# Kernel optimization log

Measured on AMD Instinct MI355X. Metric: run time of the kernel, lower is better.

Reference implementation:

```python
import jax, jax.numpy as jnp
import numpy as np

N = 50000      # nodes
E = 1600000    # edges (avg degree 32)
D_IN = 128
HID = 64


def setup_inputs() -> dict:
    key = jax.random.key(0)
    ks = jax.random.split(key, 7)
    x = jax.random.normal(ks[0], (N, D_IN), dtype=jnp.float32)
    ei = jax.random.randint(ks[1], (2, E), 0, N, dtype=jnp.int32)
    ew = jax.random.uniform(ks[2], (E,), dtype=jnp.float32)
    # GCNConv linear weights (glorot-ish scale); lin has no bias, conv bias added post-aggregation
    W1 = jax.random.normal(ks[3], (HID, D_IN), dtype=jnp.float32) * (1.0 / np.sqrt(D_IN))
    b1 = jnp.zeros((HID,), dtype=jnp.float32)
    W2 = jax.random.normal(ks[4], (HID, HID), dtype=jnp.float32) * (1.0 / np.sqrt(HID))
    b2 = jnp.zeros((HID,), dtype=jnp.float32)
    return {"x": x, "ei": ei, "ew": ew, "W1": W1, "b1": b1, "W2": W2, "b2": b2}


def _gcn_conv(x, src, dst, ew_all, W, b, n_nodes):
    """PyG GCNConv: gcn_norm (self-loops already appended) + x@W.T, gather-scale-scatter, +b."""
    deg = jax.ops.segment_sum(ew_all, dst, num_segments=n_nodes)  # dst-side weighted degree
    dinv = jnp.where(deg > 0, jax.lax.rsqrt(deg), 0.0)            # deg^{-1/2}, inf->0
    norm = dinv[src] * ew_all * dinv[dst]                          # [E+N]
    h = x @ W.T                                                    # [N, hid]
    msg = h[src] * norm[:, None]                                   # gather + scale
    out = jax.ops.segment_sum(msg, dst, num_segments=n_nodes)     # scatter-add
    return out + b


def reference(x, ei, ew, W1, b1, W2, b2):
    n_nodes = x.shape[0]
    # add self loops once (fill value 1.0), shared by both conv layers
    loop = jnp.arange(n_nodes, dtype=ei.dtype)
    src = jnp.concatenate([ei[0], loop])
    dst = jnp.concatenate([ei[1], loop])
    ew_all = jnp.concatenate([ew, jnp.ones((n_nodes,), dtype=ew.dtype)])

    h1 = jax.nn.relu(_gcn_conv(x, src, dst, ew_all, W1, b1, n_nodes))
    # dropout is identity in eval mode
    h2 = _gcn_conv(h1, src, dst, ew_all, W2, b2, n_nodes)
    return h2 + h1
```

## Files before the change

kernel.cpp:

```cpp
#include <hip/hip_runtime.h>

#define HID 64
#define DIN 128
#define NBLK 512
#define CSH 14
#define CAP (1 << CSH)
#define PAD 68

typedef unsigned long long ull;
typedef unsigned short u16;

static __device__ __forceinline__ u16 f2bf(float f) {
  unsigned u = __float_as_uint(f);
  unsigned lsb = (u >> 16) & 1u;
  u += 0x7fffu + lsb;
  return (u16)(u >> 16);
}


template <int K, int NT, bool XT_PRELOADED>
__device__ __forceinline__ void gemm_tile(const float* __restrict__ X,
                                          const float* __restrict__ W,
                                          u16* __restrict__ out,
                                          float* XT, float* WL,
                                          int n0, int n_nodes, int tid) {
  constexpr int ROWS = NT / 8;
  const int tx = tid & 15;
  const int ty = tid >> 4;
  float acc[2][4] = {{0.f}};

  for (int ph = 0; ph < K / 64; ++ph) {
    const int d0 = ph * 64;
    __syncthreads();
    if (!XT_PRELOADED) {
#pragma unroll
      for (int k = 0; k < 2; ++k) {
        int f = tid + k * NT;
        int r = f >> 4, q = f & 15;
        int n = n0 + r;
        float4 xv = (n < n_nodes)
          ? *reinterpret_cast<const float4*>(&X[(size_t)n * K + d0 + 4 * q])
          : make_float4(0.f, 0.f, 0.f, 0.f);
        *reinterpret_cast<float4*>(&XT[r * PAD + 4 * q]) = xv;
      }
    }
#pragma unroll
    for (int k = 0; k < 1024 / NT; ++k) {
      int gq = tid + k * NT;
      int qd = gq >> 6, j = gq & 63;
      float4 wv = *reinterpret_cast<const float4*>(&W[(size_t)j * K + d0 + 4 * qd]);
      WL[(4 * qd + 0) * PAD + j] = wv.x;
      WL[(4 * qd + 1) * PAD + j] = wv.y;
      WL[(4 * qd + 2) * PAD + j] = wv.z;
      WL[(4 * qd + 3) * PAD + j] = wv.w;
    }
    __syncthreads();
#pragma unroll 4
    for (int dd = 0; dd < 64; dd += 4) {
      float4 ws[4];
#pragma unroll
      for (int dk = 0; dk < 4; ++dk)
        ws[dk] = *reinterpret_cast<const float4*>(&WL[(dd + dk) * PAD + 4 * tx]);
      float4 x0 = *reinterpret_cast<const float4*>(&XT[ty * PAD + dd]);
      float4 x1 = *reinterpret_cast<const float4*>(&XT[(ty + ROWS / 2) * PAD + dd]);
      float xm0[4] = {x0.x, x0.y, x0.z, x0.w};
      float xm1[4] = {x1.x, x1.y, x1.z, x1.w};
#pragma unroll
      for (int dk = 0; dk < 4; ++dk) {
        acc[0][0] = fmaf(xm0[dk], ws[dk].x, acc[0][0]);
        acc[0][1] = fmaf(xm0[dk], ws[dk].y, acc[0][1]);
        acc[0][2] = fmaf(xm0[dk], ws[dk].z, acc[0][2]);
        acc[0][3] = fmaf(xm0[dk], ws[dk].w, acc[0][3]);
        acc[1][0] = fmaf(xm1[dk], ws[dk].x, acc[1][0]);
        acc[1][1] = fmaf(xm1[dk], ws[dk].y, acc[1][1]);
        acc[1][2] = fmaf(xm1[dk], ws[dk].z, acc[1][2]);
        acc[1][3] = fmaf(xm1[dk], ws[dk].w, acc[1][3]);
      }
    }
  }

#pragma unroll
  for (int mi = 0; mi < 2; ++mi) {
    int n = n0 + mi * (ROWS / 2) + ty;
    if (n < n_nodes) {
      ushort4 o = make_ushort4(f2bf(acc[mi][0]), f2bf(acc[mi][1]),
                               f2bf(acc[mi][2]), f2bf(acc[mi][3]));
      *reinterpret_cast<ushort4*>(&out[(size_t)n * HID + 4 * tx]) = o;
    }
  }
}


__global__ __launch_bounds__(512) void k_build_gemm(const int* __restrict__ src,
                                                    const int* __restrict__ dst,
                                                    const float* __restrict__ ew,
                                                    int* __restrict__ cursor,
                                                    int2* __restrict__ bufA,
                                                    int E, int chunk,
                                                    const float* __restrict__ x,
                                                    const float* __restrict__ W1,
                                                    u16* __restrict__ h,
                                                    int n_nodes) {
  __shared__ float S[2 * 64 * PAD];
  int b = blockIdx.x, tid = threadIdx.x;
  if (b >= NBLK) {
    gemm_tile<DIN, 512, false>(x, W1, h, S, S + 64 * PAD, (b - NBLK) * 64, n_nodes, tid);
    return;
  }
  int* h0   = (int*)S;
  int* h1_  = (int*)S + 256;
  int* cur0 = (int*)S + 512;
  int* cur1 = (int*)S + 768;
  if (tid < 256) { h0[tid] = 0; h1_[tid] = 0; }
  __syncthreads();
  int e0 = b * chunk, e1 = min(E, e0 + chunk);
  const int half = tid >> 8;
  int* hh = half ? h1_ : h0;
  int4 s4[2], d4[2];
  float4 w4[2];
  bool val[2];
#pragma unroll
  for (int it = 0; it < 2; ++it) {
    int e = e0 + 4 * tid + it * 2048;
    val[it] = (e < e1);
    if (val[it]) {
      s4[it] = *reinterpret_cast<const int4*>(&src[e]);
      d4[it] = *reinterpret_cast<const int4*>(&dst[e]);
      w4[it] = *reinterpret_cast<const float4*>(&ew[e]);
      atomicAdd(&hh[d4[it].x >> 8], 1);
      atomicAdd(&hh[d4[it].y >> 8], 1);
      atomicAdd(&hh[d4[it].z >> 8], 1);
      atomicAdd(&hh[d4[it].w >> 8], 1);
    }
  }
  for (int e = e0 + 4096 + 4 * tid; e < e1; e += 2048) {
    int4 dd = *reinterpret_cast<const int4*>(&dst[e]);
    atomicAdd(&hh[dd.x >> 8], 1);
    atomicAdd(&hh[dd.y >> 8], 1);
    atomicAdd(&hh[dd.z >> 8], 1);
    atomicAdd(&hh[dd.w >> 8], 1);
  }
  __syncthreads();
  if (tid < 256) {
    int c0 = h0[tid], c1 = h1_[tid], tot = c0 + c1;
    int ofs = (tot > 0) ? atomicAdd(&cursor[tid], tot) : 0;
    cur0[tid] = (tid << CSH) + ofs;
    cur1[tid] = (tid << CSH) + ofs + c0;
  }
  __syncthreads();
  int* cc = half ? cur1 : cur0;
#pragma unroll
  for (int it = 0; it < 2; ++it) {
    if (val[it]) {
      int p0 = atomicAdd(&cc[d4[it].x >> 8], 1);
      bufA[p0] = make_int2(__float_as_int(w4[it].x),
                           (int)(((unsigned)s4[it].x << 16) | (unsigned)d4[it].x));
      int p1 = atomicAdd(&cc[d4[it].y >> 8], 1);
      bufA[p1] = make_int2(__float_as_int(w4[it].y),
                           (int)(((unsigned)s4[it].y << 16) | (unsigned)d4[it].y));
      int p2 = atomicAdd(&cc[d4[it].z >> 8], 1);
      bufA[p2] = make_int2(__float_as_int(w4[it].z),
                           (int)(((unsigned)s4[it].z << 16) | (unsigned)d4[it].z));
      int p3 = atomicAdd(&cc[d4[it].w >> 8], 1);
      bufA[p3] = make_int2(__float_as_int(w4[it].w),
                           (int)(((unsigned)s4[it].w << 16) | (unsigned)d4[it].w));
    }
  }
  for (int e = e0 + 4096 + 4 * tid; e < e1; e += 2048) {
    int4 ss = *reinterpret_cast<const int4*>(&src[e]);
    int4 dd = *reinterpret_cast<const int4*>(&dst[e]);
    float4 ww = *reinterpret_cast<const float4*>(&ew[e]);
    int p0 = atomicAdd(&cc[dd.x >> 8], 1);
    bufA[p0] = make_int2(__float_as_int(ww.x), (int)(((unsigned)ss.x << 16) | (unsigned)dd.x));
    int p1 = atomicAdd(&cc[dd.y >> 8], 1);
    bufA[p1] = make_int2(__float_as_int(ww.y), (int)(((unsigned)ss.y << 16) | (unsigned)dd.y));
    int p2 = atomicAdd(&cc[dd.z >> 8], 1);
    bufA[p2] = make_int2(__float_as_int(ww.z), (int)(((unsigned)ss.z << 16) | (unsigned)dd.z));
    int p3 = atomicAdd(&cc[dd.w >> 8], 1);
    bufA[p3] = make_int2(__float_as_int(ww.w), (int)(((unsigned)ss.w << 16) | (unsigned)dd.w));
  }
}


__global__ __launch_bounds__(1024) void k_passB(const int2* __restrict__ bufA,
                                                const int* __restrict__ cursor,
                                                int2* __restrict__ bufB,
                                                int* __restrict__ offs,
                                                int* __restrict__ cnt,
                                                float* __restrict__ dinv,
                                                int NBC, int N) {
  int bin = blockIdx.x, tid = threadIdx.x;
  __shared__ int h2[256];
  __shared__ int cur[256];
  __shared__ float dg[256];
  int bbase = bin << CSH;
  int m = cursor[bin];
  if (tid < 256) { h2[tid] = 0; dg[tid] = 0.f; }
  __syncthreads();
  int2 rloc[16];
#pragma unroll
  for (int k = 0; k < 16; ++k) {
    int i = tid + k * 1024;
    if (i < m) {
      rloc[k] = bufA[bbase + i];
      atomicAdd(&h2[(unsigned)rloc[k].y & 255u], 1);
    }
  }
  __syncthreads();
  int own = (tid < 256) ? h2[tid] : 0;
  for (int o = 1; o < 256; o <<= 1) {
    int u = 0;
    if (tid < 256 && tid >= o) u = h2[tid - o];
    __syncthreads();
    if (tid < 256) h2[tid] += u;
    __syncthreads();
  }
  int nd = (bin << 8) + tid;
  if (tid < 256) {
    int excl = h2[tid] - own;
    cur[tid] = excl;
    if (nd < N) { offs[nd] = bbase + excl; cnt[nd] = own; }
  }
  __syncthreads();
#pragma unroll
  for (int k = 0; k < 16; ++k) {
    int i = tid + k * 1024;
    if (i < m) {
      int2 r = rloc[k];
      unsigned sd = (unsigned)r.y;
      int dl = (int)(sd & 255u);
      int p = atomicAdd(&cur[dl], 1);
      bufB[bbase + p] = make_int2(r.x, (int)(sd >> 16));
      atomicAdd(&dg[dl], __int_as_float(r.x));
    }
  }
  __syncthreads();
  if (tid < 256 && nd < N) dinv[nd] = rsqrtf(1.0f + dg[tid]);
}


__device__ __forceinline__ void bfma8(const uint4& v, float w, float* a) {
  a[0] = fmaf(__uint_as_float(v.x << 16), w, a[0]);
  a[1] = fmaf(__uint_as_float(v.x & 0xffff0000u), w, a[1]);
  a[2] = fmaf(__uint_as_float(v.y << 16), w, a[2]);
  a[3] = fmaf(__uint_as_float(v.y & 0xffff0000u), w, a[3]);
  a[4] = fmaf(__uint_as_float(v.z << 16), w, a[4]);
  a[5] = fmaf(__uint_as_float(v.z & 0xffff0000u), w, a[5]);
  a[6] = fmaf(__uint_as_float(v.w << 16), w, a[6]);
  a[7] = fmaf(__uint_as_float(v.w & 0xffff0000u), w, a[7]);
}

__device__ __forceinline__ void agg_node(const u16* __restrict__ h,
                                         const int2* __restrict__ recs,
                                         const float* __restrict__ dinv,
                                         int beg, int end, int node, float di,
                                         int lane, int p8, float* r) {
  float a[8], b[8];
  {
    uint4 v = *reinterpret_cast<const uint4*>(&h[(size_t)node * HID + p8]);
    a[0] = __uint_as_float(v.x << 16) * di;
    a[1] = __uint_as_float(v.x & 0xffff0000u) * di;
    a[2] = __uint_as_float(v.y << 16) * di;
    a[3] = __uint_as_float(v.y & 0xffff0000u) * di;
    a[4] = __uint_as_float(v.z << 16) * di;
    a[5] = __uint_as_float(v.z & 0xffff0000u) * di;
    a[6] = __uint_as_float(v.w << 16) * di;
    a[7] = __uint_as_float(v.w & 0xffff0000u) * di;
#pragma unroll
    for (int j = 0; j < 8; ++j) b[j] = 0.f;
  }

  const int gb = lane & 56;
  const int l7 = lane & 7;
  int i = beg;
  if (i + 8 <= end) {
    ull rr = *reinterpret_cast<const ull*>(&recs[i + l7]);
    float dv = dinv[(int)(rr >> 32)];
    for (;;) {
      float wd = __uint_as_float((unsigned)rr) * dv;
      ull ru = (rr & 0xffffffff00000000ull) | (ull)__float_as_uint(wd);
      bool more = (i + 16 <= end);
      ull rr_n = 0; float dv_n = 0.f;
      if (more) {
        rr_n = *reinterpret_cast<const ull*>(&recs[i + 8 + l7]);
        dv_n = dinv[(int)(rr_n >> 32)];
      }
#pragma unroll
      for (int k = 0; k < 8; ++k) {
        ull q = __shfl(ru, gb | k, 64);
        float wk = __uint_as_float((unsigned)q);
        int sk = (int)(q >> 32);
        uint4 vk = *reinterpret_cast<const uint4*>(&h[(size_t)sk * HID + p8]);
        bfma8(vk, wk, (k & 1) ? b : a);
      }
      i += 8;
      if (!more) break;
      rr = rr_n; dv = dv_n;
    }
  }
  if (i + 4 <= end) {
    int2 r0 = recs[i];     int2 r1 = recs[i + 1];
    int2 r2 = recs[i + 2]; int2 r3 = recs[i + 3];
    uint4 v0 = *reinterpret_cast<const uint4*>(&h[(size_t)r0.y * HID + p8]);
    uint4 v1 = *reinterpret_cast<const uint4*>(&h[(size_t)r1.y * HID + p8]);
    uint4 v2 = *reinterpret_cast<const uint4*>(&h[(size_t)r2.y * HID + p8]);
    uint4 v3 = *reinterpret_cast<const uint4*>(&h[(size_t)r3.y * HID + p8]);
    bfma8(v0, __int_as_float(r0.x) * dinv[r0.y], a);
    bfma8(v1, __int_as_float(r1.x) * dinv[r1.y], b);
    bfma8(v2, __int_as_float(r2.x) * dinv[r2.y], a);
    bfma8(v3, __int_as_float(r3.x) * dinv[r3.y], b);
    i += 4;
  }
  if (i + 2 <= end) {
    int2 r0 = recs[i];     int2 r1 = recs[i + 1];
    uint4 v0 = *reinterpret_cast<const uint4*>(&h[(size_t)r0.y * HID + p8]);
    uint4 v1 = *reinterpret_cast<const uint4*>(&h[(size_t)r1.y * HID + p8]);
    bfma8(v0, __int_as_float(r0.x) * dinv[r0.y], a);
    bfma8(v1, __int_as_float(r1.x) * dinv[r1.y], b);
    i += 2;
  }
  if (i < end) {
    int2 r0 = recs[i];
    uint4 v0 = *reinterpret_cast<const uint4*>(&h[(size_t)r0.y * HID + p8]);
    bfma8(v0, __int_as_float(r0.x) * dinv[r0.y], a);
  }
#pragma unroll
  for (int j = 0; j < 8; ++j) r[j] = (a[j] + b[j]) * di;
}


__global__ __launch_bounds__(256) void k_agg_gemm(const u16* __restrict__ h,
                                                  const int2* __restrict__ recs,
                                                  const int* __restrict__ offs,
                                                  const int* __restrict__ cnt,
                                                  const float* __restrict__ dinv,
                                                  const float* __restrict__ bias,
                                                  const float* __restrict__ W2,
                                                  float* __restrict__ h1,
                                                  u16* __restrict__ h2,
                                                  int n_nodes) {
  __shared__ float S[(32 + 64) * PAD];
  float* XT = S;
  float* WL = S + 32 * PAD;
  int tid = threadIdx.x;
  int lane = tid & 63;
  int p8 = (lane & 7) * 8;
  int nl = (tid >> 6) * 8 + (lane >> 3);
  int node = blockIdx.x * 32 + nl;
  if (node < n_nodes) {
    float di = dinv[node];
    float r[8];
    agg_node(h, recs, dinv, offs[node], offs[node] + cnt[node], node, di,
             lane, p8, r);
    float4 bb0 = *reinterpret_cast<const float4*>(&bias[p8]);
    float4 bb1 = *reinterpret_cast<const float4*>(&bias[p8 + 4]);
    r[0] += bb0.x; r[1] += bb0.y; r[2] += bb0.z; r[3] += bb0.w;
    r[4] += bb1.x; r[5] += bb1.y; r[6] += bb1.z; r[7] += bb1.w;
#pragma unroll
    for (int j = 0; j < 8; ++j) r[j] = fmaxf(r[j], 0.f);
    float4 lo = make_float4(r[0], r[1], r[2], r[3]);
    float4 hi = make_float4(r[4], r[5], r[6], r[7]);
    *reinterpret_cast<float4*>(&h1[(size_t)node * HID + p8]) = lo;
    *reinterpret_cast<float4*>(&h1[(size_t)node * HID + p8 + 4]) = hi;
    *reinterpret_cast<float4*>(&XT[nl * PAD + p8]) = lo;
    *reinterpret_cast<float4*>(&XT[nl * PAD + p8 + 4]) = hi;
  }
  gemm_tile<HID, 256, true>(nullptr, W2, h2, XT, WL, blockIdx.x * 32, n_nodes, tid);
}


__global__ __launch_bounds__(256) void k_agg2(const u16* __restrict__ h,
                                              const int2* __restrict__ recs,
                                              const int* __restrict__ offs,
                                              const int* __restrict__ cnt,
                                              const float* __restrict__ dinv,
                                              const float* __restrict__ bias,
                                              const float* __restrict__ resid,
                                              float* __restrict__ out, int n_nodes) {
  int tid = threadIdx.x;
  int lane = tid & 63;
  int p8 = (lane & 7) * 8;
  int node = (blockIdx.x * 4 + (tid >> 6)) * 8 + (lane >> 3);
  if (node >= n_nodes) return;
  float di = dinv[node];
  float r[8];
  agg_node(h, recs, dinv, offs[node], offs[node] + cnt[node], node, di,
           lane, p8, r);
  float4 bb0 = *reinterpret_cast<const float4*>(&bias[p8]);
  float4 bb1 = *reinterpret_cast<const float4*>(&bias[p8 + 4]);
  float4 rs0 = *reinterpret_cast<const float4*>(&resid[(size_t)node * HID + p8]);
  float4 rs1 = *reinterpret_cast<const float4*>(&resid[(size_t)node * HID + p8 + 4]);
  r[0] += bb0.x + rs0.x; r[1] += bb0.y + rs0.y;
  r[2] += bb0.z + rs0.z; r[3] += bb0.w + rs0.w;
  r[4] += bb1.x + rs1.x; r[5] += bb1.y + rs1.y;
  r[6] += bb1.z + rs1.z; r[7] += bb1.w + rs1.w;
  *reinterpret_cast<float4*>(&out[(size_t)node * HID + p8]) =
      make_float4(r[0], r[1], r[2], r[3]);
  *reinterpret_cast<float4*>(&out[(size_t)node * HID + p8 + 4]) =
      make_float4(r[4], r[5], r[6], r[7]);
}


extern "C" void kernel_launch(void* const* d_in, const int* in_sizes, int n_in,
                              void* d_out, int out_size, void* d_ws, size_t ws_size,
                              hipStream_t stream) {
  const float* x  = (const float*)d_in[0];
  const int*   ei = (const int*)d_in[1];
  const float* ew = (const float*)d_in[2];
  const float* W1 = (const float*)d_in[3];
  const float* b1 = (const float*)d_in[4];
  const float* W2 = (const float*)d_in[5];
  const float* b2 = (const float*)d_in[6];
  float* out = (float*)d_out;

  const int N = in_sizes[0] / DIN;
  const int E = in_sizes[2];
  const int* src = ei;
  const int* dst = ei + E;

  const int NBC = (N + 255) >> 8;
  const int chunk = (((E + NBLK - 1) / NBLK) + 3) & ~3;
  const int nslab = NBC << CSH;

  char* p = (char*)d_ws;
  auto carve = [&](size_t bytes) {
    char* r = p;
    p += (bytes + 255) & ~(size_t)255;
    return r;
  };
  int*   cursor = (int*)carve(256 * 4);
  int*   offs   = (int*)carve((size_t)N * 4);
  int*   cnt    = (int*)carve((size_t)N * 4);
  float* dinv   = (float*)carve((size_t)N * 4);
  int2*  bufA   = (int2*)carve((size_t)nslab * 8);
  int2*  bufB   = (int2*)carve((size_t)nslab * 8);
  u16*   h      = (u16*)carve((size_t)N * HID * 2);
  u16*   h2     = (u16*)carve((size_t)N * HID * 2);
  float* h1     = (float*)carve((size_t)N * HID * 4);

  int gblk  = (N + 63) / 64;
  int gblk2 = (N + 31) / 32;
  int ablk  = (N + 31) / 32;

  hipMemsetAsync(cursor, 0, 256 * 4, stream);
  k_build_gemm<<<NBLK + gblk, 512, 0, stream>>>(src, dst, ew, cursor, bufA, E, chunk,
                                                x, W1, h, N);
  k_passB<<<NBC, 1024, 0, stream>>>(bufA, cursor, bufB, offs, cnt, dinv, NBC, N);
  k_agg_gemm<<<gblk2, 256, 0, stream>>>(h, bufB, offs, cnt, dinv, b1, W2, h1, h2, N);
  k_agg2<<<ablk, 256, 0, stream>>>(h2, bufB, offs, cnt, dinv, b2, h1, out, N);
}
```

Baseline: 209.9 us.

## Stage bucketed edge scatter through LDS for coalesced global writes

The build kernel now sorts each block's first 4096 edges by coarse bucket in shared memory, then writes them to bufA in contiguous runs. Edges beyond the first 4096 in a chunk fall back to per-edge global atomics. Pass B now sorts records by fine bucket in LDS in chunks of 4096 before writing bufB, so stores are coalesced instead of scattered. It also computes degrees during the histogram pass. The extra LDS passes, scans and syncs are the price paid to remove random global stores.

```diff
diff --git a/kernel.cpp b/kernel.cpp
--- a/kernel.cpp
+++ b/kernel.cpp
@@ -101,83 +101,84 @@
                                                     const float* __restrict__ W1,
                                                     u16* __restrict__ h,
                                                     int n_nodes) {
-  __shared__ float S[2 * 64 * PAD];
+  __shared__ float S[9216];
   int b = blockIdx.x, tid = threadIdx.x;
   if (b >= NBLK) {
     gemm_tile<DIN, 512, false>(x, W1, h, S, S + 64 * PAD, (b - NBLK) * 64, n_nodes, tid);
     return;
   }
-  int* h0   = (int*)S;
-  int* h1_  = (int*)S + 256;
-  int* cur0 = (int*)S + 512;
-  int* cur1 = (int*)S + 768;
-  if (tid < 256) { h0[tid] = 0; h1_[tid] = 0; }
+  int2* lbuf  = (int2*)S;
+  int*  lhist = (int*)&S[8192];
+  int*  lstart= (int*)&S[8448];
+  int*  lcur  = (int*)&S[8704];
+  int*  gofs  = (int*)&S[8960];
+  if (tid < 256) lhist[tid] = 0;
   __syncthreads();
   int e0 = b * chunk, e1 = min(E, e0 + chunk);
-  const int half = tid >> 8;
-  int* hh = half ? h1_ : h0;
+  int m = e1 - e0;
   int4 s4[2], d4[2];
   float4 w4[2];
   bool val[2];
 #pragma unroll
   for (int it = 0; it < 2; ++it) {
-    int e = e0 + 4 * tid + it * 2048;
-    val[it] = (e < e1);
+    int e = e0 + 4 * (tid + it * 512);
+    val[it] = (e < e1) && (e < e0 + 4096);
     if (val[it]) {
       s4[it] = *reinterpret_cast<const int4*>(&src[e]);
       d4[it] = *reinterpret_cast<const int4*>(&dst[e]);
       w4[it] = *reinterpret_cast<const float4*>(&ew[e]);
-      atomicAdd(&hh[d4[it].x >> 8], 1);
-      atomicAdd(&hh[d4[it].y >> 8], 1);
-      atomicAdd(&hh[d4[it].z >> 8], 1);
-      atomicAdd(&hh[d4[it].w >> 8], 1);
-    }
-  }
-  for (int e = e0 + 4096 + 4 * tid; e < e1; e += 2048) {
-    int4 dd = *reinterpret_cast<const int4*>(&dst[e]);
-    atomicAdd(&hh[dd.x >> 8], 1);
-    atomicAdd(&hh[dd.y >> 8], 1);
-    atomicAdd(&hh[dd.z >> 8], 1);
-    atomicAdd(&hh[dd.w >> 8], 1);
-  }
-  __syncthreads();
+      atomicAdd(&lhist[d4[it].x >> 8], 1);
+      atomicAdd(&lhist[d4[it].y >> 8], 1);
+      atomicAdd(&lhist[d4[it].z >> 8], 1);
+      atomicAdd(&lhist[d4[it].w >> 8], 1);
+    }
+  }
+  __syncthreads();
+  int own = (tid < 256) ? lhist[tid] : 0;
+  for (int o = 1; o < 256; o <<= 1) {
+    int u = 0;
+    if (tid < 256 && tid >= o) u = lhist[tid - o];
+    __syncthreads();
+    if (tid < 256) lhist[tid] += u;
+    __syncthreads();
+  }
   if (tid < 256) {
-    int c0 = h0[tid], c1 = h1_[tid], tot = c0 + c1;
-    int ofs = (tot > 0) ? atomicAdd(&cursor[tid], tot) : 0;
-    cur0[tid] = (tid << CSH) + ofs;
-    cur1[tid] = (tid << CSH) + ofs + c0;
-  }
-  __syncthreads();
-  int* cc = half ? cur1 : cur0;
+    int excl = lhist[tid] - own;
+    lstart[tid] = excl;
+    lcur[tid] = excl;
+    int g = (own > 0) ? atomicAdd(&cursor[tid], own) : 0;
+    gofs[tid] = (tid << CSH) + g - excl;
+  }
+  __syncthreads();
 #pragma unroll
   for (int it = 0; it < 2; ++it) {
     if (val[it]) {
-      int p0 = atomicAdd(&cc[d4[it].x >> 8], 1);
-      bufA[p0] = make_int2(__float_as_int(w4[it].x),
+      int p0 = atomicAdd(&lcur[d4[it].x >> 8], 1);
+      lbuf[p0] = make_int2(__float_as_int(w4[it].x),
                            (int)(((unsigned)s4[it].x << 16) | (unsigned)d4[it].x));
-      int p1 = atomicAdd(&cc[d4[it].y >> 8], 1);
-      bufA[p1] = make_int2(__float_as_int(w4[it].y),
+      int p1 = atomicAdd(&lcur[d4[it].y >> 8], 1);
+      lbuf[p1] = make_int2(__float_as_int(w4[it].y),
                            (int)(((unsigned)s4[it].y << 16) | (unsigned)d4[it].y));
-      int p2 = atomicAdd(&cc[d4[it].z >> 8], 1);
-      bufA[p2] = make_int2(__float_as_int(w4[it].z),
+      int p2 = atomicAdd(&lcur[d4[it].z >> 8], 1);
+      lbuf[p2] = make_int2(__float_as_int(w4[it].z),
                            (int)(((unsigned)s4[it].z << 16) | (unsigned)d4[it].z));
-      int p3 = atomicAdd(&cc[d4[it].w >> 8], 1);
-      bufA[p3] = make_int2(__float_as_int(w4[it].w),
+      int p3 = atomicAdd(&lcur[d4[it].w >> 8], 1);
+      lbuf[p3] = make_int2(__float_as_int(w4[it].w),
                            (int)(((unsigned)s4[it].w << 16) | (unsigned)d4[it].w));
     }
   }
-  for (int e = e0 + 4096 + 4 * tid; e < e1; e += 2048) {
-    int4 ss = *reinterpret_cast<const int4*>(&src[e]);
-    int4 dd = *reinterpret_cast<const int4*>(&dst[e]);
-    float4 ww = *reinterpret_cast<const float4*>(&ew[e]);
-    int p0 = atomicAdd(&cc[dd.x >> 8], 1);
-    bufA[p0] = make_int2(__float_as_int(ww.x), (int)(((unsigned)ss.x << 16) | (unsigned)dd.x));
-    int p1 = atomicAdd(&cc[dd.y >> 8], 1);
-    bufA[p1] = make_int2(__float_as_int(ww.y), (int)(((unsigned)ss.y << 16) | (unsigned)dd.y));
-    int p2 = atomicAdd(&cc[dd.z >> 8], 1);
-    bufA[p2] = make_int2(__float_as_int(ww.z), (int)(((unsigned)ss.z << 16) | (unsigned)dd.z));
-    int p3 = atomicAdd(&cc[dd.w >> 8], 1);
-    bufA[p3] = make_int2(__float_as_int(ww.w), (int)(((unsigned)ss.w << 16) | (unsigned)dd.w));
+  __syncthreads();
+  int mc = min(m, 4096);
+  for (int j = tid; j < mc; j += 512) {
+    int2 r = lbuf[j];
+    int bkt = (int)(((unsigned)r.y & 0xffffu) >> 8);
+    bufA[gofs[bkt] + j] = r;
+  }
+  for (int e = e0 + 4096 + tid; e < e1; e += 512) {
+    int s = src[e], d = dst[e];
+    int g = atomicAdd(&cursor[d >> 8], 1);
+    bufA[((d >> 8) << CSH) + g] = make_int2(__float_as_int(ew[e]),
+                                            (int)(((unsigned)s << 16) | (unsigned)d));
   }
 }
 
@@ -189,13 +190,17 @@
                                                 int* __restrict__ cnt,
                                                 float* __restrict__ dinv,
                                                 int NBC, int N) {
+  __shared__ int2 sbuf[4096];
+  __shared__ int h2[256];
+  __shared__ int exf[256];
+  __shared__ int wr[256];
+  __shared__ int cst[257];
+  __shared__ int ccur[256];
+  __shared__ float dg[256];
   int bin = blockIdx.x, tid = threadIdx.x;
-  __shared__ int h2[256];
-  __shared__ int cur[256];
-  __shared__ float dg[256];
   int bbase = bin << CSH;
   int m = cursor[bin];
-  if (tid < 256) { h2[tid] = 0; dg[tid] = 0.f; }
+  if (tid < 256) { h2[tid] = 0; dg[tid] = 0.f; wr[tid] = 0; }
   __syncthreads();
   int2 rloc[16];
 #pragma unroll
@@ -203,7 +208,9 @@
     int i = tid + k * 1024;
     if (i < m) {
       rloc[k] = bufA[bbase + i];
-      atomicAdd(&h2[(unsigned)rloc[k].y & 255u], 1);
+      int fb = (int)((unsigned)rloc[k].y & 255u);
+      atomicAdd(&h2[fb], 1);
+      atomicAdd(&dg[fb], __int_as_float(rloc[k].x));
     }
   }
   __syncthreads();
@@ -218,24 +225,72 @@
   int nd = (bin << 8) + tid;
   if (tid < 256) {
     int excl = h2[tid] - own;
-    cur[tid] = excl;
-    if (nd < N) { offs[nd] = bbase + excl; cnt[nd] = own; }
-  }
-  __syncthreads();
-#pragma unroll
-  for (int k = 0; k < 16; ++k) {
-    int i = tid + k * 1024;
-    if (i < m) {
-      int2 r = rloc[k];
+    exf[tid] = excl;
+    if (nd < N) {
+      offs[nd] = bbase + excl;
+      cnt[nd] = own;
+      dinv[nd] = rsqrtf(1.0f + dg[tid]);
+    }
+  }
+  __syncthreads();
+  for (int c = 0; c < 4; ++c) {
+    int mm = m - c * 4096;
+    mm = (mm < 0) ? 0 : ((mm > 4096) ? 4096 : mm);
+    if (tid < 256) ccur[tid] = 0;
+    __syncthreads();
+    if (mm > 0) {
+#pragma unroll
+      for (int kk = 0; kk < 4; ++kk) {
+        int k = 4 * c + kk;
+        int i = tid + k * 1024;
+        if (i < m) atomicAdd(&ccur[(unsigned)rloc[k].y & 255u], 1);
+      }
+    }
+    __syncthreads();
+    if (tid < 64) {
+      int l = tid;
+      int b0 = ccur[4 * l], b1 = ccur[4 * l + 1],
+          b2 = ccur[4 * l + 2], b3 = ccur[4 * l + 3];
+      int tot = b0 + b1 + b2 + b3;
+      int inc = tot;
+      for (int o = 1; o < 64; o <<= 1) {
+        int u = __shfl_up(inc, o, 64);
+        if (l >= o) inc += u;
+      }
+      int pre = inc - tot;
+      cst[4 * l] = pre;
+      cst[4 * l + 1] = pre + b0;
+      cst[4 * l + 2] = pre + b0 + b1;
+      cst[4 * l + 3] = pre + b0 + b1 + b2;
+      if (l == 63) cst[256] = inc;
+    }
+    __syncthreads();
+    if (tid < 256) ccur[tid] = cst[tid];
+    __syncthreads();
+    if (mm > 0) {
+#pragma unroll
+      for (int kk = 0; kk < 4; ++kk) {
+        int k = 4 * c + kk;
+        int i = tid + k * 1024;
+        if (i < m) {
+          int fb = (int)((unsigned)rloc[k].y & 255u);
+          int p = atomicAdd(&ccur[fb], 1);
+          sbuf[p] = rloc[k];
+        }
+      }
+    }
+    __syncthreads();
+    for (int j = tid; j < mm; j += 1024) {
+      int2 r = sbuf[j];
       unsigned sd = (unsigned)r.y;
-      int dl = (int)(sd & 255u);
-      int p = atomicAdd(&cur[dl], 1);
-      bufB[bbase + p] = make_int2(r.x, (int)(sd >> 16));
-      atomicAdd(&dg[dl], __int_as_float(r.x));
-    }
-  }
-  __syncthreads();
-  if (tid < 256 && nd < N) dinv[nd] = rsqrtf(1.0f + dg[tid]);
+      int fb = (int)(sd & 255u);
+      int slot = bbase + exf[fb] + wr[fb] + (j - cst[fb]);
+      bufB[slot] = make_int2(r.x, (int)(sd >> 16));
+    }
+    __syncthreads();
+    if (tid < 256) wr[tid] += cst[tid + 1] - cst[tid];
+    __syncthreads();
+  }
 }
 
 
```

Result: no change. 212.4 us (+1.2%).
